# Performance work log

Hardware: AMD Instinct MI355X
Metric: run time of the kernel (lower is better)

## Reference

```python
import jax, jax.numpy as jnp
import numpy as np
from jax import lax

TIME_DECAY = 0.1  # time_decay_factor
NEG = -1e30


def setup_inputs() -> dict:
    key = jax.random.key(0)
    ks = jax.random.split(key, 6)
    B, E, N, R, D = 512, 262144, 20000, 256, 128
    return {
        "entity_index": jax.random.randint(ks[0], (B,), 0, N),
        "edge_src": jax.random.randint(ks[1], (E,), 0, N),
        "edge_dst": jax.random.randint(ks[2], (E,), 0, N),
        "edge_types": jax.random.randint(ks[3], (E,), 0, R),
        "edge_times": jax.random.uniform(ks[4], (E,), dtype=jnp.float32),
        "query_weight": jax.random.normal(ks[5], (R, D), dtype=jnp.float32),
        "k": 10,
        "num_nodes": N,
    }


def reference(entity_index, edge_src, edge_dst, edge_types, edge_times, query_weight, k, num_nodes):
    # Vectorized HICS strategy (TypeGAT.hics_strategy).
    B = entity_index.shape[0]
    R, D = query_weight.shape
    k_half = k // 2

    valid = (entity_index >= 0) & (entity_index < num_nodes)  # [B]
    # incidence masks [B, E] (same dense masks the torch code builds)
    inc_mask = edge_dst[None, :] == entity_index[:, None]
    out_mask = edge_src[None, :] == entity_index[:, None]
    inc_count = inc_mask.sum(axis=1)
    out_count = out_mask.sum(axis=1)
    has_neighbors = (inc_count > 0) | (out_count > 0)

    # topk over edge_times restricted to each entity's neighbor edges
    inc_w = jnp.where(inc_mask, edge_times[None, :], NEG)
    out_w = jnp.where(out_mask, edge_times[None, :], NEG)
    _, inc_idx = lax.top_k(inc_w, k_half)  # [B, k//2]
    _, out_idx = lax.top_k(out_w, k)       # [B, k]

    # data-dependent sample sizes, matching torch control flow
    inc_take = jnp.minimum(k_half, inc_count)                 # min(k//2, #incoming)
    remaining = jnp.where(inc_take > 0, k - inc_take, k)      # k - len(inc) if inc else k
    out_take = jnp.minimum(remaining, out_count)
    inc_valid = jnp.arange(k_half)[None, :] < inc_take[:, None]
    out_valid = jnp.arange(k)[None, :] < out_take[:, None]

    # relation-embedding gather + masked mean aggregate
    inc_embs = query_weight[edge_types[inc_idx]]  # [B, k//2, D]
    out_embs = query_weight[edge_types[out_idx]]  # [B, k, D]
    summed = (inc_embs * inc_valid[..., None].astype(inc_embs.dtype)).sum(axis=1) \
           + (out_embs * out_valid[..., None].astype(out_embs.dtype)).sum(axis=1)
    cnt = (inc_take + out_take).astype(summed.dtype)
    agg = summed / jnp.maximum(cnt, 1.0)[:, None]

    # virtual-relation fallback for no-neighbor / invalid entities
    no_neighbor = (~has_neighbors) | (~valid)
    vkey = jax.random.key(42)
    virtual_rels = jax.random.randint(vkey, (B,), 0, R)
    virtual = query_weight[virtual_rels] * jnp.exp(jnp.asarray(-TIME_DECAY, summed.dtype))

    return jnp.where(no_neighbor[:, None], virtual, agg)
```

## Files before the change

kernel.cpp:

```cpp
#include <hip/hip_runtime.h>
#include <limits.h>
#include <math.h>


#define CAP  256
#define MAXK 16

__global__ void init_kernel(int* __restrict__ table, int* __restrict__ inc_cnt,
                            int* __restrict__ out_cnt, const int* __restrict__ n_ptr, int B)
{
    const int N = n_ptr[0];
    const int stride = gridDim.x * blockDim.x;
    for (int i = blockIdx.x * blockDim.x + threadIdx.x; i < N; i += stride)
        table[i] = -1;
    for (int i = blockIdx.x * blockDim.x + threadIdx.x; i < B; i += stride) {
        inc_cnt[i] = 0;
        out_cnt[i] = 0;
    }
}

__global__ void chain_kernel(const int* __restrict__ entity_index, int* __restrict__ table,
                             int* __restrict__ next, const int* __restrict__ n_ptr, int B)
{
    const int N = n_ptr[0];
    const int b = blockIdx.x * blockDim.x + threadIdx.x;
    if (b >= B) return;
    const int e = entity_index[b];
    if (e < 0 || e >= N) { next[b] = -1; return; }
    next[b] = atomicExch(&table[e], b);
}

__global__ __launch_bounds__(256) void scan_kernel(
    const int*   __restrict__ edge_src,
    const int*   __restrict__ edge_dst,
    const float* __restrict__ edge_times,
    const int*   __restrict__ table,
    const int*   __restrict__ next,
    int* __restrict__ inc_cnt, int* __restrict__ out_cnt,
    unsigned long long* __restrict__ inc_key,
    unsigned long long* __restrict__ out_key,
    int E)
{
    const int stride = gridDim.x * blockDim.x;
    const int nvec   = E >> 2;
    const int4* src4 = (const int4*)edge_src;
    const int4* dst4 = (const int4*)edge_dst;

    for (int v = blockIdx.x * blockDim.x + threadIdx.x; v < nvec; v += stride) {
        const int4 s4 = src4[v];
        const int4 d4 = dst4[v];
        const int base = v << 2;
        const int ss[4] = { s4.x, s4.y, s4.z, s4.w };
        const int dd[4] = { d4.x, d4.y, d4.z, d4.w };
        #pragma unroll
        for (int j = 0; j < 4; ++j) {
            const int i = base + j;
            int bb = table[dd[j]];
            if (bb != -1) {
                const unsigned long long key =
                    ((unsigned long long)__float_as_uint(edge_times[i]) << 32)
                    | (unsigned long long)(0xFFFFFFFFu - (unsigned)i);
                do {
                    const int p = atomicAdd(&inc_cnt[bb], 1);
                    if (p < CAP) inc_key[(size_t)bb * CAP + p] = key;
                    bb = next[bb];
                } while (bb != -1);
            }
            bb = table[ss[j]];
            if (bb != -1) {
                const unsigned long long key =
                    ((unsigned long long)__float_as_uint(edge_times[i]) << 32)
                    | (unsigned long long)(0xFFFFFFFFu - (unsigned)i);
                do {
                    const int p = atomicAdd(&out_cnt[bb], 1);
                    if (p < CAP) out_key[(size_t)bb * CAP + p] = key;
                    bb = next[bb];
                } while (bb != -1);
            }
        }
    }
    for (int i = (nvec << 2) + blockIdx.x * blockDim.x + threadIdx.x; i < E; i += stride) {
        const int s = edge_src[i], d = edge_dst[i];
        const unsigned long long key =
            ((unsigned long long)__float_as_uint(edge_times[i]) << 32)
            | (unsigned long long)(0xFFFFFFFFu - (unsigned)i);
        int bb = table[d];
        while (bb != -1) {
            const int p = atomicAdd(&inc_cnt[bb], 1);
            if (p < CAP) inc_key[(size_t)bb * CAP + p] = key;
            bb = next[bb];
        }
        bb = table[s];
        while (bb != -1) {
            const int p = atomicAdd(&out_cnt[bb], 1);
            if (p < CAP) out_key[(size_t)bb * CAP + p] = key;
            bb = next[bb];
        }
    }
}

__global__ __launch_bounds__(128) void agg_kernel(
    const int*   __restrict__ edge_types,
    const float* __restrict__ qw,
    const int*   __restrict__ inc_cnt, const int* __restrict__ out_cnt,
    const unsigned long long* __restrict__ inc_key,
    const unsigned long long* __restrict__ out_key,
    const int*   __restrict__ k_ptr,
    float*       __restrict__ out,
    int D)
{
    const int b    = blockIdx.x;
    const int tid  = threadIdx.x;
    const int nthr = blockDim.x;
    const int k    = k_ptr[0];
    const int kh   = k >> 1;

    __shared__ unsigned long long s_inc[CAP];
    __shared__ unsigned long long s_out[CAP];
    __shared__ int s_sel[2 * MAXK];

    const int full_in  = inc_cnt[b];
    const int full_out = out_cnt[b];
    const int c_in  = min(full_in,  CAP);
    const int c_out = min(full_out, CAP);

    const int inc_take  = min(kh, full_in);
    const int remaining = (inc_take > 0) ? (k - inc_take) : k;
    const int out_take  = min(remaining, full_out);

    for (int j = tid; j < c_in;  j += nthr) s_inc[j] = inc_key[(size_t)b * CAP + j];
    for (int j = tid; j < c_out; j += nthr) s_out[j] = out_key[(size_t)b * CAP + j];
    __syncthreads();

    for (int j = tid; j < c_in; j += nthr) {
        const unsigned long long kj = s_inc[j];
        int rank = 0;
        for (int m = 0; m < c_in; ++m) rank += (s_inc[m] > kj);
        if (rank < inc_take) {
            const int idx = (int)(0xFFFFFFFFu - (unsigned)(kj & 0xFFFFFFFFull));
            s_sel[rank] = edge_types[idx];
        }
    }
    for (int j = tid; j < c_out; j += nthr) {
        const unsigned long long kj = s_out[j];
        int rank = 0;
        for (int m = 0; m < c_out; ++m) rank += (s_out[m] > kj);
        if (rank < out_take) {
            const int idx = (int)(0xFFFFFFFFu - (unsigned)(kj & 0xFFFFFFFFull));
            s_sel[MAXK + rank] = edge_types[idx];
        }
    }
    __syncthreads();

    const int cnt = inc_take + out_take;
    const float inv = 1.0f / (float)max(cnt, 1);
    for (int d = tid; d < D; d += nthr) {
        float acc = 0.0f;
        for (int s = 0; s < inc_take; ++s) acc += qw[s_sel[s] * D + d];
        for (int s = 0; s < out_take; ++s) acc += qw[s_sel[MAXK + s] * D + d];
        out[(size_t)b * D + d] = acc * inv;
    }
}

extern "C" void kernel_launch(void* const* d_in, const int* in_sizes, int n_in,
                              void* d_out, int out_size, void* d_ws, size_t ws_size,
                              hipStream_t stream)
{
    const int*   entity_index = (const int*)d_in[0];
    const int*   edge_src     = (const int*)d_in[1];
    const int*   edge_dst     = (const int*)d_in[2];
    const int*   edge_types   = (const int*)d_in[3];
    const float* edge_times   = (const float*)d_in[4];
    const float* qw           = (const float*)d_in[5];
    const int*   k_ptr        = (const int*)d_in[6];
    const int*   n_ptr        = (const int*)d_in[7];
    float*       out          = (float*)d_out;

    const int B = in_sizes[0];
    const int E = in_sizes[1];
    const int D = out_size / B;

    char* ws = (char*)d_ws;
    size_t off = 0;
    unsigned long long* inc_key = (unsigned long long*)(ws + off); off += (size_t)B * CAP * 8;
    unsigned long long* out_key = (unsigned long long*)(ws + off); off += (size_t)B * CAP * 8;
    int* inc_cnt = (int*)(ws + off); off += (size_t)B * 4;
    int* out_cnt = (int*)(ws + off); off += (size_t)B * 4;
    int* next    = (int*)(ws + off); off += (size_t)B * 4;
    int* table   = (int*)(ws + off);

    hipLaunchKernelGGL(init_kernel, dim3(256), dim3(256), 0, stream,
                       table, inc_cnt, out_cnt, n_ptr, B);
    hipLaunchKernelGGL(chain_kernel, dim3((B + 255) / 256), dim3(256), 0, stream,
                       entity_index, table, next, n_ptr, B);
    hipLaunchKernelGGL(scan_kernel, dim3(256), dim3(256), 0, stream,
                       edge_src, edge_dst, edge_times, table, next,
                       inc_cnt, out_cnt, inc_key, out_key, E);
    hipLaunchKernelGGL(agg_kernel, dim3(B), dim3(128), 0, stream,
                       edge_types, qw, inc_cnt, out_cnt, inc_key, out_key,
                       k_ptr, out, D);
}
```

Baseline: 87.43 us.

## Fuse pipeline into cooperative kernel with per-block LDS hash of query entities

After: 153.3 us. +75.3%, slower.

```diff
diff --git a/kernel.cpp b/kernel.cpp
--- a/kernel.cpp
+++ b/kernel.cpp
@@ -1,52 +1,75 @@
 #include <hip/hip_runtime.h>
+#include <hip/hip_cooperative_groups.h>
 #include <limits.h>
-#include <math.h>
-
-
-#define CAP  256
-#define MAXK 16
-
-__global__ void init_kernel(int* __restrict__ table, int* __restrict__ inc_cnt,
-                            int* __restrict__ out_cnt, const int* __restrict__ n_ptr, int B)
-{
+
+namespace cg = cooperative_groups;
+
+
+#define CAP   64
+#define MAXK  16
+#define HSIZE 2048
+#define HMASK (HSIZE - 1)
+#define MAXB  1024
+
+
+__device__ __forceinline__ void build_hash(const int* __restrict__ entity_index,
+                                           const int* __restrict__ n_ptr, int B,
+                                           int* h_key, int* h_head, int* h_next)
+{
+    const int tid = threadIdx.x, nthr = blockDim.x;
+    for (int i = tid; i < HSIZE; i += nthr) { h_key[i] = -1; h_head[i] = -1; }
+    __syncthreads();
     const int N = n_ptr[0];
-    const int stride = gridDim.x * blockDim.x;
-    for (int i = blockIdx.x * blockDim.x + threadIdx.x; i < N; i += stride)
-        table[i] = -1;
-    for (int i = blockIdx.x * blockDim.x + threadIdx.x; i < B; i += stride) {
-        inc_cnt[i] = 0;
-        out_cnt[i] = 0;
-    }
-}
-
-__global__ void chain_kernel(const int* __restrict__ entity_index, int* __restrict__ table,
-                             int* __restrict__ next, const int* __restrict__ n_ptr, int B)
-{
-    const int N = n_ptr[0];
-    const int b = blockIdx.x * blockDim.x + threadIdx.x;
-    if (b >= B) return;
-    const int e = entity_index[b];
-    if (e < 0 || e >= N) { next[b] = -1; return; }
-    next[b] = atomicExch(&table[e], b);
-}
-
-__global__ __launch_bounds__(256) void scan_kernel(
-    const int*   __restrict__ edge_src,
-    const int*   __restrict__ edge_dst,
+    for (int b = tid; b < B; b += nthr) {
+        const int e = entity_index[b];
+        if (e < 0 || e >= N) continue;
+        int s = e & HMASK;
+        for (;;) {
+            const int prev = atomicCAS(&h_key[s], -1, e);
+            if (prev == -1 || prev == e) break;
+            s = (s + 1) & HMASK;
+        }
+        h_next[b] = atomicExch(&h_head[s], b);
+    }
+    __syncthreads();
+}
+
+__device__ __forceinline__ int hash_lookup(const int* h_key, const int* h_head, int e)
+{
+    int s = e & HMASK;
+    for (;;) {
+        const int kk = h_key[s];
+        if (kk == e)  return h_head[s];
+        if (kk == -1) return -1;
+        s = (s + 1) & HMASK;
+    }
+}
+
+__device__ __forceinline__ void push_chain(int head, unsigned long long key,
+                                           const int* h_next, int* cnt,
+                                           unsigned long long* keybuf)
+{
+    for (int bb = head; bb != -1; bb = h_next[bb]) {
+        const int p = atomicAdd(&cnt[bb], 1);
+        if (p < CAP) keybuf[(size_t)bb * CAP + p] = key;
+    }
+}
+
+__device__ __forceinline__ void scan_edges_lds(
+    const int* __restrict__ edge_src, const int* __restrict__ edge_dst,
     const float* __restrict__ edge_times,
-    const int*   __restrict__ table,
-    const int*   __restrict__ next,
+    const int* h_key, const int* h_head, const int* h_next,
     int* __restrict__ inc_cnt, int* __restrict__ out_cnt,
     unsigned long long* __restrict__ inc_key,
-    unsigned long long* __restrict__ out_key,
-    int E)
-{
-    const int stride = gridDim.x * blockDim.x;
-    const int nvec   = E >> 2;
+    unsigned long long* __restrict__ out_key, int E)
+{
+    const int gid  = blockIdx.x * blockDim.x + threadIdx.x;
+    const int gstr = gridDim.x * blockDim.x;
+    const int nvec = E >> 2;
     const int4* src4 = (const int4*)edge_src;
     const int4* dst4 = (const int4*)edge_dst;
 
-    for (int v = blockIdx.x * blockDim.x + threadIdx.x; v < nvec; v += stride) {
+    for (int v = gid; v < nvec; v += gstr) {
         const int4 s4 = src4[v];
         const int4 d4 = dst4[v];
         const int base = v << 2;
@@ -55,31 +78,157 @@
         #pragma unroll
         for (int j = 0; j < 4; ++j) {
             const int i = base + j;
-            int bb = table[dd[j]];
-            if (bb != -1) {
+            const int hin  = hash_lookup(h_key, h_head, dd[j]);
+            const int hout = hash_lookup(h_key, h_head, ss[j]);
+            if ((hin | hout) != -2) {
+            }
+            if (hin != -1 || hout != -1) {
                 const unsigned long long key =
                     ((unsigned long long)__float_as_uint(edge_times[i]) << 32)
                     | (unsigned long long)(0xFFFFFFFFu - (unsigned)i);
-                do {
-                    const int p = atomicAdd(&inc_cnt[bb], 1);
-                    if (p < CAP) inc_key[(size_t)bb * CAP + p] = key;
-                    bb = next[bb];
-                } while (bb != -1);
+                if (hin  != -1) push_chain(hin,  key, h_next, inc_cnt, inc_key);
+                if (hout != -1) push_chain(hout, key, h_next, out_cnt, out_key);
             }
-            bb = table[ss[j]];
-            if (bb != -1) {
-                const unsigned long long key =
-                    ((unsigned long long)__float_as_uint(edge_times[i]) << 32)
-                    | (unsigned long long)(0xFFFFFFFFu - (unsigned)i);
-                do {
-                    const int p = atomicAdd(&out_cnt[bb], 1);
-                    if (p < CAP) out_key[(size_t)bb * CAP + p] = key;
-                    bb = next[bb];
-                } while (bb != -1);
-            }
-        }
-    }
-    for (int i = (nvec << 2) + blockIdx.x * blockDim.x + threadIdx.x; i < E; i += stride) {
+        }
+    }
+    for (int i = (nvec << 2) + gid; i < E; i += gstr) {
+        const int hin  = hash_lookup(h_key, h_head, edge_dst[i]);
+        const int hout = hash_lookup(h_key, h_head, edge_src[i]);
+        if (hin != -1 || hout != -1) {
+            const unsigned long long key =
+                ((unsigned long long)__float_as_uint(edge_times[i]) << 32)
+                | (unsigned long long)(0xFFFFFFFFu - (unsigned)i);
+            if (hin  != -1) push_chain(hin,  key, h_next, inc_cnt, inc_key);
+            if (hout != -1) push_chain(hout, key, h_next, out_cnt, out_key);
+        }
+    }
+}
+
+__device__ __forceinline__ void agg_one(int b,
+    const int* __restrict__ edge_types, const float* __restrict__ qw,
+    const int* __restrict__ inc_cnt, const int* __restrict__ out_cnt,
+    const unsigned long long* __restrict__ inc_key,
+    const unsigned long long* __restrict__ out_key,
+    int k, float* __restrict__ outp, int D,
+    unsigned long long* s_inc, unsigned long long* s_out, int* s_sel)
+{
+    const int tid = threadIdx.x, nthr = blockDim.x;
+    const int kh = k >> 1;
+
+    __syncthreads();
+
+    const int full_in  = inc_cnt[b];
+    const int full_out = out_cnt[b];
+    const int c_in  = min(full_in,  CAP);
+    const int c_out = min(full_out, CAP);
+    const int inc_take  = min(kh, full_in);
+    const int remaining = (inc_take > 0) ? (k - inc_take) : k;
+    const int out_take  = min(remaining, full_out);
+
+    for (int j = tid; j < c_in;  j += nthr) s_inc[j] = inc_key[(size_t)b * CAP + j];
+    for (int j = tid; j < c_out; j += nthr) s_out[j] = out_key[(size_t)b * CAP + j];
+    __syncthreads();
+
+    for (int j = tid; j < c_in; j += nthr) {
+        const unsigned long long kj = s_inc[j];
+        int rank = 0;
+        for (int m = 0; m < c_in; ++m) rank += (s_inc[m] > kj);
+        if (rank < inc_take)
+            s_sel[rank] = edge_types[(int)(0xFFFFFFFFu - (unsigned)(kj & 0xFFFFFFFFull))];
+    }
+    for (int j = tid; j < c_out; j += nthr) {
+        const unsigned long long kj = s_out[j];
+        int rank = 0;
+        for (int m = 0; m < c_out; ++m) rank += (s_out[m] > kj);
+        if (rank < out_take)
+            s_sel[MAXK + rank] = edge_types[(int)(0xFFFFFFFFu - (unsigned)(kj & 0xFFFFFFFFull))];
+    }
+    __syncthreads();
+
+    const int cnt = inc_take + out_take;
+    const float inv = 1.0f / (float)max(cnt, 1);
+    for (int d = tid; d < D; d += nthr) {
+        float acc = 0.0f;
+        for (int s = 0; s < inc_take; ++s) acc += qw[s_sel[s] * D + d];
+        for (int s = 0; s < out_take; ++s) acc += qw[s_sel[MAXK + s] * D + d];
+        outp[(size_t)b * D + d] = acc * inv;
+    }
+}
+
+
+__global__ __launch_bounds__(256) void fused_kernel(
+    const int*   __restrict__ entity_index,
+    const int*   __restrict__ edge_src,
+    const int*   __restrict__ edge_dst,
+    const float* __restrict__ edge_times,
+    const int*   __restrict__ edge_types,
+    const float* __restrict__ qw,
+    const int*   __restrict__ k_ptr,
+    const int*   __restrict__ n_ptr,
+    int*         __restrict__ cnts,
+    unsigned long long* __restrict__ inc_key,
+    unsigned long long* __restrict__ out_key,
+    float*       __restrict__ outp,
+    int B, int E, int D)
+{
+    __shared__ int h_key[HSIZE];
+    __shared__ int h_head[HSIZE];
+    __shared__ int h_next[MAXB];
+    __shared__ unsigned long long s_inc[CAP];
+    __shared__ unsigned long long s_out[CAP];
+    __shared__ int s_sel[2 * MAXK];
+
+    const int gid  = blockIdx.x * blockDim.x + threadIdx.x;
+    const int gstr = gridDim.x * blockDim.x;
+
+    for (int i = gid; i < 2 * B; i += gstr) cnts[i] = 0;
+    build_hash(entity_index, n_ptr, B, h_key, h_head, h_next);
+    cg::this_grid().sync();
+
+    scan_edges_lds(edge_src, edge_dst, edge_times, h_key, h_head, h_next,
+                   cnts, cnts + B, inc_key, out_key, E);
+    cg::this_grid().sync();
+
+    const int k = k_ptr[0];
+    for (int b = blockIdx.x; b < B; b += gridDim.x)
+        agg_one(b, edge_types, qw, cnts, cnts + B, inc_key, out_key,
+                k, outp, D, s_inc, s_out, s_sel);
+}
+
+
+__global__ void fb_init(int* __restrict__ table, int* __restrict__ cnts,
+                        const int* __restrict__ n_ptr, int B)
+{
+    const int N = n_ptr[0];
+    const int stride = gridDim.x * blockDim.x;
+    for (int i = blockIdx.x * blockDim.x + threadIdx.x; i < N; i += stride)
+        table[i] = -1;
+    for (int i = blockIdx.x * blockDim.x + threadIdx.x; i < 2 * B; i += stride)
+        cnts[i] = 0;
+}
+
+__global__ void fb_chain(const int* __restrict__ entity_index, int* __restrict__ table,
+                         int* __restrict__ next, const int* __restrict__ n_ptr, int B)
+{
+    const int N = n_ptr[0];
+    const int b = blockIdx.x * blockDim.x + threadIdx.x;
+    if (b >= B) return;
+    const int e = entity_index[b];
+    if (e < 0 || e >= N) { next[b] = -1; return; }
+    next[b] = atomicExch(&table[e], b);
+}
+
+__global__ __launch_bounds__(256) void fb_scan(
+    const int* __restrict__ edge_src, const int* __restrict__ edge_dst,
+    const float* __restrict__ edge_times,
+    const int* __restrict__ table, const int* __restrict__ next,
+    int* __restrict__ inc_cnt, int* __restrict__ out_cnt,
+    unsigned long long* __restrict__ inc_key,
+    unsigned long long* __restrict__ out_key, int E)
+{
+    const int gid  = blockIdx.x * blockDim.x + threadIdx.x;
+    const int gstr = gridDim.x * blockDim.x;
+    for (int i = gid; i < E; i += gstr) {
         const int s = edge_src[i], d = edge_dst[i];
         const unsigned long long key =
             ((unsigned long long)__float_as_uint(edge_times[i]) << 32)
@@ -99,68 +248,20 @@
     }
 }
 
-__global__ __launch_bounds__(128) void agg_kernel(
-    const int*   __restrict__ edge_types,
-    const float* __restrict__ qw,
-    const int*   __restrict__ inc_cnt, const int* __restrict__ out_cnt,
+__global__ __launch_bounds__(128) void fb_agg(
+    const int* __restrict__ edge_types, const float* __restrict__ qw,
+    const int* __restrict__ inc_cnt, const int* __restrict__ out_cnt,
     const unsigned long long* __restrict__ inc_key,
     const unsigned long long* __restrict__ out_key,
-    const int*   __restrict__ k_ptr,
-    float*       __restrict__ out,
-    int D)
-{
-    const int b    = blockIdx.x;
-    const int tid  = threadIdx.x;
-    const int nthr = blockDim.x;
-    const int k    = k_ptr[0];
-    const int kh   = k >> 1;
-
+    const int* __restrict__ k_ptr, float* __restrict__ outp, int D)
+{
     __shared__ unsigned long long s_inc[CAP];
     __shared__ unsigned long long s_out[CAP];
     __shared__ int s_sel[2 * MAXK];
-
-    const int full_in  = inc_cnt[b];
-    const int full_out = out_cnt[b];
-    const int c_in  = min(full_in,  CAP);
-    const int c_out = min(full_out, CAP);
-
-    const int inc_take  = min(kh, full_in);
-    const int remaining = (inc_take > 0) ? (k - inc_take) : k;
-    const int out_take  = min(remaining, full_out);
-
-    for (int j = tid; j < c_in;  j += nthr) s_inc[j] = inc_key[(size_t)b * CAP + j];
-    for (int j = tid; j < c_out; j += nthr) s_out[j] = out_key[(size_t)b * CAP + j];
-    __syncthreads();
-
-    for (int j = tid; j < c_in; j += nthr) {
-        const unsigned long long kj = s_inc[j];
-        int rank = 0;
-        for (int m = 0; m < c_in; ++m) rank += (s_inc[m] > kj);
-        if (rank < inc_take) {
-            const int idx = (int)(0xFFFFFFFFu - (unsigned)(kj & 0xFFFFFFFFull));
-            s_sel[rank] = edge_types[idx];
-        }
-    }
-    for (int j = tid; j < c_out; j += nthr) {
-        const unsigned long long kj = s_out[j];
-        int rank = 0;
-        for (int m = 0; m < c_out; ++m) rank += (s_out[m] > kj);
-        if (rank < out_take) {
-            const int idx = (int)(0xFFFFFFFFu - (unsigned)(kj & 0xFFFFFFFFull));
-            s_sel[MAXK + rank] = edge_types[idx];
-        }
-    }
-    __syncthreads();
-
-    const int cnt = inc_take + out_take;
-    const float inv = 1.0f / (float)max(cnt, 1);
-    for (int d = tid; d < D; d += nthr) {
-        float acc = 0.0f;
-        for (int s = 0; s < inc_take; ++s) acc += qw[s_sel[s] * D + d];
-        for (int s = 0; s < out_take; ++s) acc += qw[s_sel[MAXK + s] * D + d];
-        out[(size_t)b * D + d] = acc * inv;
-    }
-}
+    agg_one(blockIdx.x, edge_types, qw, inc_cnt, out_cnt, inc_key, out_key,
+            k_ptr[0], outp, D, s_inc, s_out, s_sel);
+}
+
 
 extern "C" void kernel_launch(void* const* d_in, const int* in_sizes, int n_in,
                               void* d_out, int out_size, void* d_ws, size_t ws_size,
@@ -174,29 +275,44 @@
     const float* qw           = (const float*)d_in[5];
     const int*   k_ptr        = (const int*)d_in[6];
     const int*   n_ptr        = (const int*)d_in[7];
-    float*       out          = (float*)d_out;
-
-    const int B = in_sizes[0];
-    const int E = in_sizes[1];
-    const int D = out_size / B;
+    float*       outp         = (float*)d_out;
+
+    int B = in_sizes[0];
+    int E = in_sizes[1];
+    int D = out_size / B;
 
     char* ws = (char*)d_ws;
-    size_t off = 0;
-    unsigned long long* inc_key = (unsigned long long*)(ws + off); off += (size_t)B * CAP * 8;
-    unsigned long long* out_key = (unsigned long long*)(ws + off); off += (size_t)B * CAP * 8;
-    int* inc_cnt = (int*)(ws + off); off += (size_t)B * 4;
-    int* out_cnt = (int*)(ws + off); off += (size_t)B * 4;
-    int* next    = (int*)(ws + off); off += (size_t)B * 4;
-    int* table   = (int*)(ws + off);
-
-    hipLaunchKernelGGL(init_kernel, dim3(256), dim3(256), 0, stream,
-                       table, inc_cnt, out_cnt, n_ptr, B);
-    hipLaunchKernelGGL(chain_kernel, dim3((B + 255) / 256), dim3(256), 0, stream,
-                       entity_index, table, next, n_ptr, B);
-    hipLaunchKernelGGL(scan_kernel, dim3(256), dim3(256), 0, stream,
-                       edge_src, edge_dst, edge_times, table, next,
-                       inc_cnt, out_cnt, inc_key, out_key, E);
-    hipLaunchKernelGGL(agg_kernel, dim3(B), dim3(128), 0, stream,
-                       edge_types, qw, inc_cnt, out_cnt, inc_key, out_key,
-                       k_ptr, out, D);
-}
+    unsigned long long* inc_key = (unsigned long long*)ws;
+    unsigned long long* out_key = inc_key + (size_t)B * CAP;
+    int* cnts  = (int*)(out_key + (size_t)B * CAP);
+    int* next  = cnts + 2 * (size_t)B;
+    int* table = next + (size_t)B;
+
+    bool coop_done = false;
+    if (B <= MAXB) {
+        void* args[] = {
+            (void*)&entity_index, (void*)&edge_src, (void*)&edge_dst,
+            (void*)&edge_times, (void*)&edge_types, (void*)&qw,
+            (void*)&k_ptr, (void*)&n_ptr, (void*)&cnts,
+            (void*)&inc_key, (void*)&out_key, (void*)&outp,
+            (void*)&B, (void*)&E, (void*)&D
+        };
+        hipError_t err = hipLaunchCooperativeKernel((const void*)fused_kernel,
+                                                    dim3(256), dim3(256),
+                                                    args, 0, stream);
+        coop_done = (err == hipSuccess);
+    }
+
+    if (!coop_done) {
+        hipLaunchKernelGGL(fb_init, dim3(256), dim3(256), 0, stream,
+                           table, cnts, n_ptr, B);
+        hipLaunchKernelGGL(fb_chain, dim3((B + 255) / 256), dim3(256), 0, stream,
+                           entity_index, table, next, n_ptr, B);
+        hipLaunchKernelGGL(fb_scan, dim3(256), dim3(256), 0, stream,
+                           edge_src, edge_dst, edge_times, table, next,
+                           cnts, cnts + B, inc_key, out_key, E);
+        hipLaunchKernelGGL(fb_agg, dim3(B), dim3(128), 0, stream,
+                           edge_types, qw, cnts, cnts + B, inc_key, out_key,
+                           k_ptr, outp, D);
+    }
+}
```
